# Optimization experiments

Hardware: AMD Instinct MI355X
Metric: run time of the kernel (lower is better)

The kernel has to match this reference:

```python
import jax, jax.numpy as jnp
import numpy as np

B, T, C = 2, 1024, 1024
NH, HS, BD, HORIZON = 16, 64, 16, 64


def setup_inputs() -> dict:
    key = jax.random.key(0)
    ks = jax.random.split(key, 16)
    s = 0.02
    return {
        "x": jax.random.normal(ks[0], (B, T, C), jnp.float32),
        "W_disp": jax.random.normal(ks[1], (NH * BD, C), jnp.float32) * s,
        "b_disp": jnp.zeros((NH * BD,), jnp.float32),
        "W_val": jax.random.normal(ks[2], (C, C), jnp.float32) * s,
        "b_val": jnp.zeros((C,), jnp.float32),
        "rel_pos_emb": jax.random.normal(ks[3], (HORIZON, BD), jnp.float32) * s,
        "W_fused": jax.random.normal(ks[4], (2 * BD, BD), jnp.float32) * s,
        "b_fused": jnp.zeros((2 * BD,), jnp.float32),
        "W_pos": jax.random.normal(ks[5], (BD, BD), jnp.float32) * s,
        "W_bond": jax.random.normal(ks[6], (BD,), jnp.float32) * s,
        "b_bond": jnp.zeros((), jnp.float32),
        "W_dmg": jax.random.normal(ks[7], (BD,), jnp.float32) * s,
        "b_dmg": jnp.full((), -3.0, jnp.float32),  # nn.init.constant_(damage_out.bias, -3.0)
        "W_cproj": jax.random.normal(ks[8], (C, C), jnp.float32) * s,
        "b_cproj": jnp.zeros((C,), jnp.float32),
    }


def reference(x, W_disp, b_disp, W_val, b_val, rel_pos_emb, W_fused, b_fused,
              W_pos, W_bond, b_bond, W_dmg, b_dmg, W_cproj, b_cproj):
    delta = min(HORIZON, T)
    gelu = lambda z: jax.nn.gelu(z, approximate=False)  # torch F.gelu default (erf)

    # projections + head split: (B,nh,T,bd) / (B,nh,T,hs)
    disp = (x @ W_disp.T + b_disp).reshape(B, T, NH, BD).transpose(0, 2, 1, 3)
    val = (x @ W_val.T + b_val).reshape(B, T, NH, HS).transpose(0, 2, 1, 3)

    pad = delta - 1
    disp_pad = jnp.pad(disp, ((0, 0), (0, 0), (pad, 0), (0, 0)))
    idx = jnp.arange(T)[:, None] + jnp.arange(delta)[None, :]  # (T,delta) into padded axis
    disp_win = disp_pad[:, :, idx]                      # (B,nh,T,delta,bd)
    strain = disp_win - disp[:, :, :, None, :]          # bond strain

    fused = strain @ W_fused.T + b_fused                # (B,nh,T,delta,2bd)
    bond_f, dmg_f = fused[..., :BD], fused[..., BD:]
    pos_feat = rel_pos_emb[:delta] @ W_pos.T            # (delta,bd)

    bond_logits = gelu(bond_f + pos_feat) @ W_bond + b_bond          # (B,nh,T,delta)
    damage = jax.nn.sigmoid(gelu(dmg_f) @ W_dmg + b_dmg)             # (B,nh,T,delta)
    logits = bond_logits - 10.0 * damage

    cmask = (jnp.arange(T)[:, None] - delta + 1 + jnp.arange(delta)[None, :]) >= 0
    logits = jnp.where(cmask[None, None], logits, -jnp.inf)
    weights = jax.nn.softmax(logits, axis=-1)           # (B,nh,T,delta)

    # weighted sum over window without materializing (B,nh,T,delta,hs)
    val_pad = jnp.pad(val, ((0, 0), (0, 0), (pad, 0), (0, 0)))
    def body(acc, j):
        sl = jax.lax.dynamic_slice_in_dim(val_pad, j, T, axis=2)  # (B,nh,T,hs)
        return acc + weights[..., j][..., None] * sl, None
    out0 = jnp.zeros((B, NH, T, HS), jnp.float32)
    out, _ = jax.lax.scan(body, out0, jnp.arange(delta))

    y = out.transpose(0, 2, 1, 3).reshape(B, T, C)
    return y @ W_cproj.T + b_cproj
```

## Files before the change

kernel.cpp:

```cpp
#include <hip/hip_runtime.h>

#define BDIM 16
#define HSZ 64
#define NHEAD 16
#define DELTA 64
#define LOG2E 1.4426950408889634f

typedef __bf16 bf16x8 __attribute__((ext_vector_type(8)));
typedef float f32x4 __attribute__((ext_vector_type(4)));
typedef float f32x2 __attribute__((ext_vector_type(2)));
typedef unsigned short us8 __attribute__((ext_vector_type(8)));
typedef unsigned int u32;

__device__ __forceinline__ unsigned short f2bf(float f) {
    u32 u = __float_as_uint(f);
    return (unsigned short)((u + 0x7fffu + ((u >> 16) & 1u)) >> 16);
}

__device__ __forceinline__ void gload_lds16(const void* g, void* l) {
    __builtin_amdgcn_global_load_lds(
        (const __attribute__((address_space(1))) void*)g,
        (__attribute__((address_space(3))) void*)l, 16, 0, 0);
}

__global__ __launch_bounds__(256) void cast4_bf16(
    const float* __restrict__ s0, unsigned short* __restrict__ d0,
    const float* __restrict__ s1, unsigned short* __restrict__ d1,
    const float* __restrict__ s2, unsigned short* __restrict__ d2,
    const float* __restrict__ s3, unsigned short* __restrict__ d3,
    const float* __restrict__ bd, const float* __restrict__ bv,
    float* __restrict__ bcat) {
    int blk = blockIdx.x;
    if (blk == 4352) {
        for (int t = threadIdx.x; t < 320; t += 256) {
            if (t < 64) ((float4*)bcat)[t] = ((const float4*)bd)[t];
            else        ((float4*)bcat)[t] = ((const float4*)bv)[t - 64];
        }
        return;
    }
    const float* src; unsigned short* dst; int base;
    if (blk < 2048)      { src = s0; dst = d0; base = blk; }
    else if (blk < 2304) { src = s1; dst = d1; base = blk - 2048; }
    else if (blk < 3328) { src = s2; dst = d2; base = blk - 2304; }
    else                 { src = s3; dst = d3; base = blk - 3328; }
    int i = base * 256 + threadIdx.x;
    float4 f = ((const float4*)src)[i];
    ushort4 o;
    o.x = f2bf(f.x); o.y = f2bf(f.y); o.z = f2bf(f.z); o.w = f2bf(f.w);
    ((ushort4*)dst)[i] = o;
}

__global__ __launch_bounds__(256) void gemm_bf16(const unsigned short* __restrict__ A,
                                                 const unsigned short* __restrict__ Bw,
                                                 const float* __restrict__ bias,
                                                 float* __restrict__ C,
                                                 unsigned short* __restrict__ CbT,
                                                 int N, int K, int nbx, int mode) {
    __shared__ __align__(16) unsigned short lA[2][16 * 512];
    __shared__ __align__(16) unsigned short lB[2][8 * 512];
    int tid = threadIdx.x;
    int w = tid >> 6, lane = tid & 63;
    int id = blockIdx.x;
    int xcd = id & 7, rr = id >> 3;
    int mi = xcd * 2 + (rr & 1);
    int ni = rr >> 1;
    int bm = mi * 128, bn = ni * 64;
    int wr = w & 1, wc = w >> 1;
    int m16 = lane & 15, q = lane >> 4;

    const unsigned short* aPtr[4];
    const unsigned short* bPtr[2];
#pragma unroll
    for (int i = 0; i < 4; ++i) {
        int g = w + 4 * i;
        aPtr[i] = A + (long)(bm + (g & 7) * 16 + m16) * K + (g >> 3) * 32 + q * 8;
    }
#pragma unroll
    for (int i = 0; i < 2; ++i) {
        int g = w + 4 * i;
        bPtr[i] = Bw + (long)(bn + (g & 3) * 16 + m16) * K + (g >> 2) * 32 + q * 8;
    }

    f32x4 acc[4][2];
#pragma unroll
    for (int i = 0; i < 4; ++i)
#pragma unroll
        for (int j = 0; j < 2; ++j) acc[i][j] = (f32x4){0.f, 0.f, 0.f, 0.f};

    int nk = K >> 6;
#pragma unroll
    for (int i = 0; i < 4; ++i) gload_lds16(aPtr[i], &lA[0][(w + 4 * i) * 512]);
#pragma unroll
    for (int i = 0; i < 2; ++i) gload_lds16(bPtr[i], &lB[0][(w + 4 * i) * 512]);

    for (int kt = 0; kt < nk; ++kt) {
        int p = kt & 1;
        __syncthreads();
        if (kt + 1 < nk) {
            int ko = (kt + 1) * 64;
#pragma unroll
            for (int i = 0; i < 4; ++i)
                gload_lds16(aPtr[i] + ko, &lA[p ^ 1][(w + 4 * i) * 512]);
#pragma unroll
            for (int i = 0; i < 2; ++i)
                gload_lds16(bPtr[i] + ko, &lB[p ^ 1][(w + 4 * i) * 512]);
        }
#pragma unroll
        for (int s = 0; s < 2; ++s) {
            bf16x8 af[4], bg[2];
#pragma unroll
            for (int r = 0; r < 4; ++r)
                af[r] = *(const bf16x8*)&lA[p][(s * 8 + wr * 4 + r) * 512 + lane * 8];
#pragma unroll
            for (int n = 0; n < 2; ++n)
                bg[n] = *(const bf16x8*)&lB[p][(s * 4 + wc * 2 + n) * 512 + lane * 8];
#pragma unroll
            for (int r = 0; r < 4; ++r)
#pragma unroll
                for (int n = 0; n < 2; ++n)
                    acc[r][n] = __builtin_amdgcn_mfma_f32_16x16x32_bf16(af[r], bg[n], acc[r][n], 0, 0, 0);
        }
    }

    if (mode == 0 || bn < 256) {
        int ldc = (mode == 0) ? N : 256;
#pragma unroll
        for (int n = 0; n < 2; ++n) {
            int col = bn + wc * 32 + n * 16 + m16;
            float bv = bias[col];
#pragma unroll
            for (int r = 0; r < 4; ++r)
#pragma unroll
                for (int e = 0; e < 4; ++e) {
                    int row = bm + wr * 64 + r * 16 + q * 4 + e;
                    C[(long)row * ldc + col] = acc[r][n][e] + bv;
                }
        }
    } else {
        __syncthreads();
        unsigned short* sC = (unsigned short*)&lA[0][0];
#pragma unroll
        for (int n = 0; n < 2; ++n) {
            int col_l = wc * 32 + n * 16 + m16;
            float bv = bias[bn + col_l];
#pragma unroll
            for (int r = 0; r < 4; ++r)
#pragma unroll
                for (int e = 0; e < 4; ++e) {
                    int row_l = wr * 64 + r * 16 + q * 4 + e;
                    sC[row_l * 64 + col_l] = f2bf(acc[r][n][e] + bv);
                }
        }
        __syncthreads();
        long base0 = ((long)(bm >> 10)) * 1048576 + (long)(bn - 256) * 1024 + (bm & 1023);
#pragma unroll
        for (int it = 0; it < 4; ++it) {
            int slot = it * 256 + tid;
            int hs = (slot >> 3) & 63;
            int tc = (slot & 7) * 8 + (slot >> 9) * 64;
            us8 o;
#pragma unroll
            for (int j = 0; j < 8; ++j) o[j] = sC[(tc + j) * 64 + hs];
            *(us8*)&CbT[base0 + (long)hs * 1024 + tc] = o;
        }
    }
}

__device__ __forceinline__ f32x2 gelu2(f32x2 z) {
    f32x2 z2 = z * z;
    f32x2 u = z * (0.7978845608f + 0.0356774081f * z2);
    f32x2 u2 = u * u;
    f32x2 den = 1.f + 0.33333333f * u2;
    f32x2 r;
    r.x = __builtin_amdgcn_rcpf(den.x);
    r.y = __builtin_amdgcn_rcpf(den.y);
    f32x2 th = u * r;
    f32x2 zh = 0.5f * z;
    return zh + zh * th;
}

#define PROJ_LD 36
#define SW_LD 104

__global__ __launch_bounds__(256, 4) void attn_kernel(
    const float* __restrict__ disp,
    const unsigned short* __restrict__ valT,
    const float* __restrict__ rel,
    const float* __restrict__ Wpos,
    const float* __restrict__ Wf,
    const float* __restrict__ bfu,
    const float* __restrict__ Wb,
    const float* __restrict__ bb_p,
    const float* __restrict__ Wd,
    const float* __restrict__ bd_p,
    unsigned short* __restrict__ y,
    int T) {
    __shared__ __align__(16) unsigned short sWd[32 * SW_LD];
    __shared__ __align__(16) float ov[96 * PROJ_LD + 96 * 16 + 512];
    float* sProj = ov;
    float* sDisp = ov + 96 * PROJ_LD;
    float* sWfT  = sDisp + 96 * 16;
    unsigned short* sValT = (unsigned short*)ov;

    int tid = threadIdx.x;
    int t0 = (blockIdx.x & 31) * 32;
    int bh = blockIdx.x >> 5;
    int b = bh >> 4, h = bh & 15;
    int wave = tid >> 6, lane = tid & 63;
    int m16 = lane & 15, q = lane >> 4;

    {
        uint4 z4 = make_uint4(0, 0, 0, 0);
        for (int i = tid; i < 416; i += 256) ((uint4*)sWd)[i] = z4;
        sWfT[(tid & 15) * 32 + (tid >> 4)] = Wf[tid];
        { int j = tid + 256; sWfT[(j & 15) * 32 + (j >> 4)] = Wf[j]; }
        for (int i = tid; i < 384; i += 256) {
            int r = i >> 2, qq = i & 3;
            int ts = t0 + r - 64;
            float4 v = make_float4(0.f, 0.f, 0.f, 0.f);
            if (ts >= 0)
                v = ((const float4*)(disp + ((long)(b * T + ts) * NHEAD + h) * BDIM))[qq];
            *(float4*)&sDisp[r * 16 + qq * 4] = v;
        }
    }
    __syncthreads();
    for (int idx = tid; idx < 96 * 32; idx += 256) {
        int r = idx >> 5, k = idx & 31;
        float a = 0.f;
#pragma unroll
        for (int d = 0; d < 16; ++d) a += sDisp[r * 16 + d] * sWfT[d * 32 + k];
        sProj[r * PROJ_LD + k] = a;
    }

    float relv[16];
#pragma unroll
    for (int e = 0; e < 4; ++e) {
        float4 rr = ((const float4*)rel)[lane * 4 + e];
        relv[e * 4 + 0] = rr.x; relv[e * 4 + 1] = rr.y;
        relv[e * 4 + 2] = rr.z; relv[e * 4 + 3] = rr.w;
    }
    f32x2 pfd[16], wbd[16];
#pragma unroll
    for (int d = 0; d < 16; ++d) {
        float a = 0.f;
#pragma unroll
        for (int e = 0; e < 16; ++e) a += relv[e] * Wpos[d * 16 + e];
        pfd[d].x = a + bfu[d];
        pfd[d].y = bfu[16 + d];
        wbd[d].x = Wb[d];
        wbd[d].y = Wd[d];
    }
    float bbond = *bb_p, bdmg = *bd_p;
    __syncthreads();

    int wbase = wave * 8;
    for (int rr = 0; rr < 8; ++rr) {
        int tl = wbase + rr;
        int rs = tl + 1 + lane;
        int rc = tl + 64;
        bool valid = (t0 + tl + lane - 63) >= 0;
        float cb[16], cd[16], pb[16], pd[16];
        const float* crow = &sProj[rc * PROJ_LD];
        const float* prow = &sProj[rs * PROJ_LD];
#pragma unroll
        for (int qq = 0; qq < 4; ++qq) {
            float4 v1 = *(const float4*)&crow[qq * 4];
            float4 v2 = *(const float4*)&crow[16 + qq * 4];
            float4 v3 = *(const float4*)&prow[qq * 4];
            float4 v4 = *(const float4*)&prow[16 + qq * 4];
            cb[qq*4+0]=v1.x; cb[qq*4+1]=v1.y; cb[qq*4+2]=v1.z; cb[qq*4+3]=v1.w;
            cd[qq*4+0]=v2.x; cd[qq*4+1]=v2.y; cd[qq*4+2]=v2.z; cd[qq*4+3]=v2.w;
            pb[qq*4+0]=v3.x; pb[qq*4+1]=v3.y; pb[qq*4+2]=v3.z; pb[qq*4+3]=v3.w;
            pd[qq*4+0]=v4.x; pd[qq*4+1]=v4.y; pd[qq*4+2]=v4.z; pd[qq*4+3]=v4.w;
        }
        f32x2 acc2 = (f32x2){bbond, bdmg};
#pragma unroll
        for (int k = 0; k < 16; ++k) {
            f32x2 pz, cz;
            pz.x = pb[k]; pz.y = pd[k];
            cz.x = cb[k]; cz.y = cd[k];
            f32x2 z = pz - cz + pfd[k];
            acc2 = acc2 + gelu2(z) * wbd[k];
        }
        float bl = acc2.x, dm = acc2.y;
        float damage = __builtin_amdgcn_rcpf(1.f + __builtin_exp2f(-dm * LOG2E));
        float logit = bl - 10.f * damage;
        float e = valid ? __builtin_exp2f(logit * LOG2E) : 0.f;
        float ssum = e;
#pragma unroll
        for (int off = 32; off >= 1; off >>= 1) ssum += __shfl_xor(ssum, off);
        sWd[tl * SW_LD + rs] = f2bf(e * __builtin_amdgcn_rcpf(ssum));
    }
    __syncthreads();

    for (int i = tid; i < 768; i += 256) {
        int g = i >> 6, hs = i & 63;
        int ts0 = t0 - 64 + g * 8;
        us8 v = (us8)0;
        if (ts0 >= 0)
            v = *(const us8*)&valT[((long)(b * NHEAD * HSZ + h * HSZ + hs)) * T + ts0];
        *(us8*)&sValT[hs * SW_LD + g * 8] = v;
    }
    __syncthreads();

    {
        int mi = wave & 1;
        int nh = (wave >> 1) * 2;
        f32x4 acc[2];
#pragma unroll
        for (int n = 0; n < 2; ++n) acc[n] = (f32x4){0.f, 0.f, 0.f, 0.f};
#pragma unroll
        for (int kt = 0; kt < 3; ++kt) {
            bf16x8 a = *(const bf16x8*)&sWd[(mi * 16 + m16) * SW_LD + kt * 32 + q * 8];
#pragma unroll
            for (int n = 0; n < 2; ++n) {
                bf16x8 bv = *(const bf16x8*)&sValT[((nh + n) * 16 + m16) * SW_LD + kt * 32 + q * 8];
                acc[n] = __builtin_amdgcn_mfma_f32_16x16x32_bf16(a, bv, acc[n], 0, 0, 0);
            }
        }
        int trow = t0 + mi * 16 + q * 4;
#pragma unroll
        for (int n = 0; n < 2; ++n) {
            int col = h * HSZ + (nh + n) * 16 + m16;
#pragma unroll
            for (int e = 0; e < 4; ++e)
                y[(long)(b * T + trow + e) * (NHEAD * HSZ) + col] = f2bf(acc[n][e]);
        }
    }
}

extern "C" void kernel_launch(void* const* d_in, const int* in_sizes, int n_in,
                              void* d_out, int out_size, void* d_ws, size_t ws_size,
                              hipStream_t stream) {
    const float* x       = (const float*)d_in[0];
    const float* W_disp  = (const float*)d_in[1];
    const float* b_disp  = (const float*)d_in[2];
    const float* W_val   = (const float*)d_in[3];
    const float* b_val   = (const float*)d_in[4];
    const float* rel     = (const float*)d_in[5];
    const float* W_fused = (const float*)d_in[6];
    const float* b_fused = (const float*)d_in[7];
    const float* W_pos   = (const float*)d_in[8];
    const float* W_bond  = (const float*)d_in[9];
    const float* b_bond  = (const float*)d_in[10];
    const float* W_dmg   = (const float*)d_in[11];
    const float* b_dmg   = (const float*)d_in[12];
    const float* W_cproj = (const float*)d_in[13];
    const float* b_cproj = (const float*)d_in[14];
    float* out = (float*)d_out;
    float* ws  = (float*)d_ws;

    const int B = 2, T = 1024, C = 1024;
    float* disp = ws;
    float* bcat = disp + 524288;
    unsigned short* x_bf  = (unsigned short*)(bcat + 1280);
    unsigned short* valT  = x_bf + 2097152;
    unsigned short* Wcat  = valT + 2097152;
    unsigned short* Wv_bf = Wcat + 262144;
    unsigned short* Wc_bf = Wv_bf + 1048576;
    unsigned short* y_bf  = x_bf;

    cast4_bf16<<<4353, 256, 0, stream>>>(x, x_bf, W_disp, Wcat, W_val, Wv_bf,
                                         W_cproj, Wc_bf, b_disp, b_val, bcat);

    gemm_bf16<<<320, 256, 0, stream>>>(x_bf, Wcat, bcat, disp, valT,
                                       1280, C, 20, 1);
    attn_kernel<<<dim3(B * NHEAD * (T / 32)), 256, 0, stream>>>(
        disp, valT, rel, W_pos, W_fused, b_fused, W_bond, b_bond, W_dmg, b_dmg,
        y_bf, T);
    gemm_bf16<<<256, 256, 0, stream>>>(y_bf, Wc_bf, b_cproj, out, nullptr,
                                       C, C, 16, 0);
}
```

Measured before the change: 169.8 us.

## Fuse fp32-to-bf16 casts into first GEMM's load path, drop separate cast kernel

Removes the standalone cast kernel. The first projection GEMM now reads fp32 x and weights directly into registers, converts them to bf16 and stores them into LDS with register-level double buffering. Extra blocks in the same launch convert W_cproj for the later GEMM. This saves a kernel launch and the round trip of writing and re-reading bf16 copies of x and the weights. The cost is losing the async global-to-LDS loads, doing the conversion inside the GEMM's critical path, and each tile re-reading fp32 data at twice the bytes.

```diff
diff --git a/kernel.cpp b/kernel.cpp
--- a/kernel.cpp
+++ b/kernel.cpp
@@ -3,7 +3,6 @@
 #define BDIM 16
 #define HSZ 64
 #define NHEAD 16
-#define DELTA 64
 #define LOG2E 1.4426950408889634f
 
 typedef __bf16 bf16x8 __attribute__((ext_vector_type(8)));
@@ -23,41 +22,172 @@
         (__attribute__((address_space(3))) void*)l, 16, 0, 0);
 }
 
-__global__ __launch_bounds__(256) void cast4_bf16(
-    const float* __restrict__ s0, unsigned short* __restrict__ d0,
-    const float* __restrict__ s1, unsigned short* __restrict__ d1,
-    const float* __restrict__ s2, unsigned short* __restrict__ d2,
-    const float* __restrict__ s3, unsigned short* __restrict__ d3,
-    const float* __restrict__ bd, const float* __restrict__ bv,
-    float* __restrict__ bcat) {
-    int blk = blockIdx.x;
-    if (blk == 4352) {
-        for (int t = threadIdx.x; t < 320; t += 256) {
-            if (t < 64) ((float4*)bcat)[t] = ((const float4*)bd)[t];
-            else        ((float4*)bcat)[t] = ((const float4*)bv)[t - 64];
+__device__ __forceinline__ us8 cvt8(float4 a, float4 b) {
+    us8 o;
+    o[0] = f2bf(a.x); o[1] = f2bf(a.y); o[2] = f2bf(a.z); o[3] = f2bf(a.w);
+    o[4] = f2bf(b.x); o[5] = f2bf(b.y); o[6] = f2bf(b.z); o[7] = f2bf(b.w);
+    return o;
+}
+
+__global__ __launch_bounds__(256) void gemm1x(
+    const float* __restrict__ x,
+    const float* __restrict__ Wd,
+    const float* __restrict__ Wv,
+    const float* __restrict__ bd,
+    const float* __restrict__ bv,
+    const float* __restrict__ Wc,
+    unsigned short* __restrict__ Wc_bf,
+    float* __restrict__ disp,
+    unsigned short* __restrict__ valT) {
+    int id = blockIdx.x;
+    int tid = threadIdx.x;
+    if (id >= 320) {
+        int idx = (id - 320) * 256 + tid;
+#pragma unroll
+        for (int i = 0; i < 8; ++i) {
+            int j = idx + i * 32768;
+            float4 f = ((const float4*)Wc)[j];
+            ushort4 o;
+            o.x = f2bf(f.x); o.y = f2bf(f.y); o.z = f2bf(f.z); o.w = f2bf(f.w);
+            ((ushort4*)Wc_bf)[j] = o;
         }
         return;
     }
-    const float* src; unsigned short* dst; int base;
-    if (blk < 2048)      { src = s0; dst = d0; base = blk; }
-    else if (blk < 2304) { src = s1; dst = d1; base = blk - 2048; }
-    else if (blk < 3328) { src = s2; dst = d2; base = blk - 2304; }
-    else                 { src = s3; dst = d3; base = blk - 3328; }
-    int i = base * 256 + threadIdx.x;
-    float4 f = ((const float4*)src)[i];
-    ushort4 o;
-    o.x = f2bf(f.x); o.y = f2bf(f.y); o.z = f2bf(f.z); o.w = f2bf(f.w);
-    ((ushort4*)dst)[i] = o;
-}
-
-__global__ __launch_bounds__(256) void gemm_bf16(const unsigned short* __restrict__ A,
-                                                 const unsigned short* __restrict__ Bw,
-                                                 const float* __restrict__ bias,
-                                                 float* __restrict__ C,
-                                                 unsigned short* __restrict__ CbT,
-                                                 int N, int K, int nbx, int mode) {
     __shared__ __align__(16) unsigned short lA[2][16 * 512];
     __shared__ __align__(16) unsigned short lB[2][8 * 512];
+    const int K = 1024, nk = 16;
+    int w = tid >> 6, lane = tid & 63;
+    int xcd = id & 7, rr = id >> 3;
+    int mi = xcd * 2 + (rr & 1);
+    int ni = rr >> 1;
+    int bm = mi * 128, bn = ni * 64;
+    int wr = w & 1, wc = w >> 1;
+    int m16 = lane & 15, q = lane >> 4;
+
+    const float* aSrc[4];
+    const float* bSrc[2];
+#pragma unroll
+    for (int i = 0; i < 4; ++i) {
+        int g = w + 4 * i;
+        aSrc[i] = x + (long)(bm + (g & 7) * 16 + m16) * K + (g >> 3) * 32 + q * 8;
+    }
+#pragma unroll
+    for (int i = 0; i < 2; ++i) {
+        int g = w + 4 * i;
+        int row = bn + (g & 3) * 16 + m16;
+        bSrc[i] = (row < 256 ? Wd + (long)row * K : Wv + (long)(row - 256) * K)
+                  + (g >> 2) * 32 + q * 8;
+    }
+
+    float4 aR[4][2], bR[2][2];
+#define LOAD_REGS(kt)                                              \
+    {                                                              \
+        int ko = (kt) * 64;                                        \
+        _Pragma("unroll")                                          \
+        for (int i = 0; i < 4; ++i) {                              \
+            aR[i][0] = *(const float4*)(aSrc[i] + ko);             \
+            aR[i][1] = *(const float4*)(aSrc[i] + ko + 4);         \
+        }                                                          \
+        _Pragma("unroll")                                          \
+        for (int i = 0; i < 2; ++i) {                              \
+            bR[i][0] = *(const float4*)(bSrc[i] + ko);             \
+            bR[i][1] = *(const float4*)(bSrc[i] + ko + 4);         \
+        }                                                          \
+    }
+#define CVT_WRITE(p)                                               \
+    {                                                              \
+        _Pragma("unroll")                                          \
+        for (int i = 0; i < 4; ++i)                                \
+            *(us8*)&lA[p][(w + 4 * i) * 512 + lane * 8] = cvt8(aR[i][0], aR[i][1]); \
+        _Pragma("unroll")                                          \
+        for (int i = 0; i < 2; ++i)                                \
+            *(us8*)&lB[p][(w + 4 * i) * 512 + lane * 8] = cvt8(bR[i][0], bR[i][1]); \
+    }
+
+    f32x4 acc[4][2];
+#pragma unroll
+    for (int i = 0; i < 4; ++i)
+#pragma unroll
+        for (int j = 0; j < 2; ++j) acc[i][j] = (f32x4){0.f, 0.f, 0.f, 0.f};
+
+    LOAD_REGS(0);
+    CVT_WRITE(0);
+    LOAD_REGS(1);
+
+    for (int kt = 0; kt < nk; ++kt) {
+        int p = kt & 1;
+        __syncthreads();
+        if (kt + 1 < nk) CVT_WRITE(p ^ 1);
+        if (kt + 2 < nk) LOAD_REGS(kt + 2);
+#pragma unroll
+        for (int s = 0; s < 2; ++s) {
+            bf16x8 af[4], bg[2];
+#pragma unroll
+            for (int r = 0; r < 4; ++r)
+                af[r] = *(const bf16x8*)&lA[p][(s * 8 + wr * 4 + r) * 512 + lane * 8];
+#pragma unroll
+            for (int n = 0; n < 2; ++n)
+                bg[n] = *(const bf16x8*)&lB[p][(s * 4 + wc * 2 + n) * 512 + lane * 8];
+#pragma unroll
+            for (int r = 0; r < 4; ++r)
+#pragma unroll
+                for (int n = 0; n < 2; ++n)
+                    acc[r][n] = __builtin_amdgcn_mfma_f32_16x16x32_bf16(af[r], bg[n], acc[r][n], 0, 0, 0);
+        }
+    }
+#undef LOAD_REGS
+#undef CVT_WRITE
+
+    if (bn < 256) {
+#pragma unroll
+        for (int n = 0; n < 2; ++n) {
+            int col = bn + wc * 32 + n * 16 + m16;
+            float bvv = bd[col];
+#pragma unroll
+            for (int r = 0; r < 4; ++r)
+#pragma unroll
+                for (int e = 0; e < 4; ++e) {
+                    int row = bm + wr * 64 + r * 16 + q * 4 + e;
+                    disp[(long)row * 256 + col] = acc[r][n][e] + bvv;
+                }
+        }
+    } else {
+        __syncthreads();
+        unsigned short* sC = (unsigned short*)&lA[0][0];
+#pragma unroll
+        for (int n = 0; n < 2; ++n) {
+            int col_l = wc * 32 + n * 16 + m16;
+            float bvv = bv[bn + col_l - 256];
+#pragma unroll
+            for (int r = 0; r < 4; ++r)
+#pragma unroll
+                for (int e = 0; e < 4; ++e) {
+                    int row_l = wr * 64 + r * 16 + q * 4 + e;
+                    sC[row_l * 64 + col_l] = f2bf(acc[r][n][e] + bvv);
+                }
+        }
+        __syncthreads();
+        long base0 = ((long)(bm >> 10)) * 1048576 + (long)(bn - 256) * 1024 + (bm & 1023);
+#pragma unroll
+        for (int it = 0; it < 4; ++it) {
+            int slot = it * 256 + tid;
+            int hs = (slot >> 3) & 63;
+            int tc = (slot & 7) * 8 + (slot >> 9) * 64;
+            us8 o;
+#pragma unroll
+            for (int j = 0; j < 8; ++j) o[j] = sC[(tc + j) * 64 + hs];
+            *(us8*)&valT[base0 + (long)hs * 1024 + tc] = o;
+        }
+    }
+}
+
+__global__ __launch_bounds__(256) void gemm2(const unsigned short* __restrict__ A,
+                                             const unsigned short* __restrict__ Bw,
+                                             const float* __restrict__ bias,
+                                             float* __restrict__ C) {
+    __shared__ __align__(16) unsigned short lA[2][16 * 512];
+    __shared__ __align__(16) unsigned short lB[2][8 * 512];
+    const int K = 1024, N = 1024, nk = 16;
     int tid = threadIdx.x;
     int w = tid >> 6, lane = tid & 63;
     int id = blockIdx.x;
@@ -87,7 +217,6 @@
 #pragma unroll
         for (int j = 0; j < 2; ++j) acc[i][j] = (f32x4){0.f, 0.f, 0.f, 0.f};
 
-    int nk = K >> 6;
 #pragma unroll
     for (int i = 0; i < 4; ++i) gload_lds16(aPtr[i], &lA[0][(w + 4 * i) * 512]);
 #pragma unroll
@@ -122,47 +251,17 @@
         }
     }
 
-    if (mode == 0 || bn < 256) {
-        int ldc = (mode == 0) ? N : 256;
-#pragma unroll
-        for (int n = 0; n < 2; ++n) {
-            int col = bn + wc * 32 + n * 16 + m16;
-            float bv = bias[col];
-#pragma unroll
-            for (int r = 0; r < 4; ++r)
-#pragma unroll
-                for (int e = 0; e < 4; ++e) {
-                    int row = bm + wr * 64 + r * 16 + q * 4 + e;
-                    C[(long)row * ldc + col] = acc[r][n][e] + bv;
-                }
-        }
-    } else {
-        __syncthreads();
-        unsigned short* sC = (unsigned short*)&lA[0][0];
-#pragma unroll
-        for (int n = 0; n < 2; ++n) {
-            int col_l = wc * 32 + n * 16 + m16;
-            float bv = bias[bn + col_l];
-#pragma unroll
-            for (int r = 0; r < 4; ++r)
-#pragma unroll
-                for (int e = 0; e < 4; ++e) {
-                    int row_l = wr * 64 + r * 16 + q * 4 + e;
-                    sC[row_l * 64 + col_l] = f2bf(acc[r][n][e] + bv);
-                }
-        }
-        __syncthreads();
-        long base0 = ((long)(bm >> 10)) * 1048576 + (long)(bn - 256) * 1024 + (bm & 1023);
-#pragma unroll
-        for (int it = 0; it < 4; ++it) {
-            int slot = it * 256 + tid;
-            int hs = (slot >> 3) & 63;
-            int tc = (slot & 7) * 8 + (slot >> 9) * 64;
-            us8 o;
-#pragma unroll
-            for (int j = 0; j < 8; ++j) o[j] = sC[(tc + j) * 64 + hs];
-            *(us8*)&CbT[base0 + (long)hs * 1024 + tc] = o;
-        }
+#pragma unroll
+    for (int n = 0; n < 2; ++n) {
+        int col = bn + wc * 32 + n * 16 + m16;
+        float bvv = bias[col];
+#pragma unroll
+        for (int r = 0; r < 4; ++r)
+#pragma unroll
+            for (int e = 0; e < 4; ++e) {
+                int row = bm + wr * 64 + r * 16 + q * 4 + e;
+                C[(long)row * N + col] = acc[r][n][e] + bvv;
+            }
     }
 }
 
@@ -350,24 +449,16 @@
     float* out = (float*)d_out;
     float* ws  = (float*)d_ws;
 
-    const int B = 2, T = 1024, C = 1024;
+    const int B = 2, T = 1024;
     float* disp = ws;
-    float* bcat = disp + 524288;
-    unsigned short* x_bf  = (unsigned short*)(bcat + 1280);
-    unsigned short* valT  = x_bf + 2097152;
-    unsigned short* Wcat  = valT + 2097152;
-    unsigned short* Wv_bf = Wcat + 262144;
-    unsigned short* Wc_bf = Wv_bf + 1048576;
-    unsigned short* y_bf  = x_bf;
-
-    cast4_bf16<<<4353, 256, 0, stream>>>(x, x_bf, W_disp, Wcat, W_val, Wv_bf,
-                                         W_cproj, Wc_bf, b_disp, b_val, bcat);
-
-    gemm_bf16<<<320, 256, 0, stream>>>(x_bf, Wcat, bcat, disp, valT,
-                                       1280, C, 20, 1);
+    unsigned short* valT  = (unsigned short*)(disp + 524288);
+    unsigned short* y_bf  = valT + 2097152;
+    unsigned short* Wc_bf = y_bf + 2097152;
+
+    gemm1x<<<448, 256, 0, stream>>>(x, W_disp, W_val, b_disp, b_val,
+                                    W_cproj, Wc_bf, disp, valT);
     attn_kernel<<<dim3(B * NHEAD * (T / 32)), 256, 0, stream>>>(
         disp, valT, rel, W_pos, W_fused, b_fused, W_bond, b_bond, W_dmg, b_dmg,
         y_bf, T);
-    gemm_bf16<<<256, 256, 0, stream>>>(y_bf, Wc_bf, b_cproj, out, nullptr,
-                                       C, C, 16, 0);
-}
+    gemm2<<<256, 256, 0, stream>>>(y_bf, Wc_bf, b_cproj, out);
+}
```

Measured after the change: 182.9 us. 1.08x slower.
